# Kernel tuning notes

Measured on AMD Instinct MI355X. Metric: run time of the kernel, lower is better.

## Reference

```python
import jax, jax.numpy as jnp
import numpy as np

D_MODEL, N_HEADS, D_HEAD, N_CTX, BATCH = 1024, 16, 64, 2048, 4
SCALED = True
NEG = 1e10


def setup_inputs() -> dict:
    key = jax.random.key(0)
    k1, k2, k3, k4 = jax.random.split(key, 4)
    s = 1.0 / np.sqrt(D_MODEL)
    return {
        "x": jax.random.normal(k1, (BATCH, N_CTX, D_MODEL), dtype=jnp.float32),
        "W_K": jax.random.normal(k2, (N_HEADS, D_HEAD, D_MODEL), dtype=jnp.float32) * s,
        "W_Q": jax.random.normal(k3, (N_HEADS, D_HEAD, D_MODEL), dtype=jnp.float32) * s,
        "W_V": jax.random.normal(k4, (N_HEADS, D_HEAD, D_MODEL), dtype=jnp.float32) * s,
    }


def reference(x, W_K, W_Q, W_V):
    b, p, _ = x.shape
    k = jnp.einsum('ihd,bpd->biph', W_K, x)
    q = jnp.einsum('ihd,bpd->biph', W_Q, x)
    v = jnp.einsum('ihd,bpd->biph', W_V, x)
    # attn_scores_pre: [b, i, q, p] (query axis named q, key axis p)
    scores = jnp.einsum('biph,biqh->biqp', k, q)
    mask = jnp.tril(jnp.ones((p, p), dtype=scores.dtype))
    scores = jnp.tril(scores) - NEG * (1.0 - mask)
    if SCALED:
        scores = scores / np.sqrt(D_HEAD)
    attn = jax.nn.softmax(scores, axis=-1)
    z = jnp.einsum('biph,biqp->biqh', v, attn)  # [b, i, q, h]
    out = jnp.transpose(z, (0, 2, 1, 3)).reshape(b, p, -1)  # b q (i h)
    return out
```

## Files before the change

kernel.cpp:

```cpp
#include <hip/hip_runtime.h>
#include <stdint.h>

typedef unsigned short u16;
typedef short bf16x8 __attribute__((ext_vector_type(8)));
typedef float f32x4 __attribute__((ext_vector_type(4)));
typedef u16 u16x8 __attribute__((ext_vector_type(8)));
typedef u16 u16x4 __attribute__((ext_vector_type(4)));
typedef uint32_t u32x2 __attribute__((ext_vector_type(2)));

#define NB 4
#define NH 16
#define NP 2048
#define NDM 1024
#define KLOG2E 0.18033688011112042f

__device__ __forceinline__ u16 f2bf(float f) {
    union { float f; uint32_t u; } v; v.f = f;
    return (u16)((v.u + 0x7FFFu + ((v.u >> 16) & 1u)) >> 16);
}

__device__ __forceinline__ uint32_t cvtpk_bf16(float lo, float hi) {
    uint32_t r;
    asm("v_cvt_pk_bf16_f32 %0, %1, %2" : "=v"(r) : "v"(lo), "v"(hi));
    return r;
}

__global__ void convert_all(const float* __restrict__ x, const float* __restrict__ wq,
                            const float* __restrict__ wk, const float* __restrict__ wv,
                            u16* __restrict__ x_bf, u16* __restrict__ w_bf) {
    const int XT = NB * NP * NDM;
    const int M1 = NDM * NDM;
    int i = (blockIdx.x * blockDim.x + threadIdx.x) * 4;
    const float* src; u16* dst; float scale = 1.0f;
    if (i < XT) { src = x + i; dst = x_bf + i; }
    else {
        int j = i - XT;
        dst = w_bf + j;
        if (j < M1)          { src = wq + j;          scale = KLOG2E; }
        else if (j < 2 * M1) { src = wk + (j - M1); }
        else                 { src = wv + (j - 2 * M1); }
    }
    float4 f = *(const float4*)src;
    u16x4 o = { f2bf(f.x * scale), f2bf(f.y * scale), f2bf(f.z * scale), f2bf(f.w * scale) };
    *(u16x4*)dst = o;
}

__device__ __forceinline__ void load_lds16(const void* g, void* l) {
    __builtin_amdgcn_global_load_lds(
        (const __attribute__((address_space(1))) uint32_t*)g,
        (__attribute__((address_space(3))) uint32_t*)l,
        16, 0, 0);
}

__global__ __launch_bounds__(256) void proj_gemm(
    const u16* __restrict__ xbf, const u16* __restrict__ wbf,
    u16* __restrict__ qws, u16* __restrict__ kws, u16* __restrict__ vT)
{
    __shared__ u16 As[128 * 64];
    __shared__ u16 Bs[128 * 64];
    int tid = threadIdx.x;
    int wave = tid >> 6, lane = tid & 63;
    int g = lane >> 4, c = lane & 15;
    int wr = wave >> 1, wc = wave & 1;
    int gx = blockIdx.x, gy = blockIdx.y;
    int wsel = gy >> 3;
    int n0 = (gy & 7) * 128;
    long m0 = (long)gx * 128;
    const u16* asrc0 = xbf + m0 * 1024;
    const u16* bsrc0 = wbf + (long)wsel * (1024 * 1024) + (long)n0 * 1024;

    int lrow = lane >> 3;
    int lcol = (lane & 7) * 8;

    f32x4 acc[4][4];
    #pragma unroll
    for (int i = 0; i < 4; i++)
        #pragma unroll
        for (int j = 0; j < 4; j++) acc[i][j] = (f32x4){0.f, 0.f, 0.f, 0.f};

    for (int kt = 0; kt < 16; kt++) {
        const u16* ak = asrc0 + kt * 64;
        const u16* bk_ = bsrc0 + kt * 64;
        #pragma unroll
        for (int r = 0; r < 4; r++) {
            int ldsoff = r * 2048 + wave * 512;
            int grow = r * 32 + wave * 8 + lrow;
            load_lds16(ak + (long)grow * 1024 + lcol, &As[ldsoff]);
            load_lds16(bk_ + (long)grow * 1024 + lcol, &Bs[ldsoff]);
        }
        __syncthreads();
        #pragma unroll
        for (int ks = 0; ks < 2; ks++) {
            bf16x8 af[4], bf_[4];
            #pragma unroll
            for (int mt = 0; mt < 4; mt++)
                af[mt] = *(const bf16x8*)&As[(wr * 64 + mt * 16 + c) * 64 + ks * 32 + g * 8];
            #pragma unroll
            for (int nt = 0; nt < 4; nt++)
                bf_[nt] = *(const bf16x8*)&Bs[(wc * 64 + nt * 16 + c) * 64 + ks * 32 + g * 8];
            #pragma unroll
            for (int mt = 0; mt < 4; mt++)
                #pragma unroll
                for (int nt = 0; nt < 4; nt++)
                    acc[mt][nt] = __builtin_amdgcn_mfma_f32_16x16x32_bf16(bf_[nt], af[mt], acc[mt][nt], 0, 0, 0);
        }
        __syncthreads();
    }

    if (wsel < 2) {
        u16* dst = (wsel == 0) ? qws : kws;
        #pragma unroll
        for (int mt = 0; mt < 4; mt++) {
            #pragma unroll
            for (int nt = 0; nt < 4; nt++) {
                long m = m0 + wr * 64 + mt * 16 + c;
                int n_base = n0 + wc * 64 + nt * 16 + g * 4;
                int b = (int)(m >> 11), p = (int)(m & 2047);
                int hd = n_base >> 6, h = n_base & 63;
                u16x4 o;
                #pragma unroll
                for (int r = 0; r < 4; r++) o[r] = f2bf(acc[mt][nt][r]);
                *(u16x4*)(dst + ((((long)b * NH + hd) * NP + p) << 6) + h) = o;
            }
        }
    } else {
        #pragma unroll
        for (int mt = 0; mt < 4; mt++) {
            long m = m0 + wr * 64 + mt * 16 + c;
            int b = (int)(m >> 11), p = (int)(m & 2047);
            #pragma unroll
            for (int nt = 0; nt < 4; nt++) {
                int n_base = n0 + wc * 64 + nt * 16 + g * 4;
                #pragma unroll
                for (int r = 0; r < 4; r++)
                    vT[((long)b * 1024 + n_base + r) * NP + p] = f2bf(acc[mt][nt][r]);
            }
        }
    }
}

template<bool MASK>
__device__ __forceinline__ void attn_tile(
    int kv0, const u16* __restrict__ kp, const u16* __restrict__ vp,
    const bf16x8 (&aq)[2][2], uint8_t* PwB, int c, int g, int sx, int q0,
    f32x4 (&acc_o)[2][4], float (&lrow)[2])
{
    float ps[2] = {0.f, 0.f};
    #pragma unroll
    for (int a = 0; a < 4; a++) {
        const u16* kr = kp + (size_t)(kv0 + a * 16 + c) * 64 + g * 8;
        bf16x8 kf0 = *(const bf16x8*)(kr);
        bf16x8 kf1 = *(const bf16x8*)(kr + 32);
        #pragma unroll
        for (int mt = 0; mt < 2; mt++) {
            f32x4 z = (f32x4){0.f, 0.f, 0.f, 0.f};
            z = __builtin_amdgcn_mfma_f32_16x16x32_bf16(kf0, aq[mt][0], z, 0, 0, 0);
            z = __builtin_amdgcn_mfma_f32_16x16x32_bf16(kf1, aq[mt][1], z, 0, 0, 0);
            float p[4];
            #pragma unroll
            for (int r = 0; r < 4; r++) {
                p[r] = __builtin_amdgcn_exp2f(z[r] - 8.0f);
                if (MASK) {
                    int key = kv0 + a * 16 + g * 4 + r;
                    int qq = q0 + mt * 16 + c;
                    if (key > qq) p[r] = 0.f;
                }
                ps[mt] += p[r];
            }
            u32x2 wd = { cvtpk_bf16(p[0], p[1]), cvtpk_bf16(p[2], p[3]) };
            *(u32x2*)(PwB + (mt * 16 + c) * 128 + ((a * 32 + g * 8) ^ sx)) = wd;
        }
    }

    bf16x8 bv0[4];
    #pragma unroll
    for (int j = 0; j < 4; j++)
        bv0[j] = *(const bf16x8*)(vp + (size_t)(j * 16 + c) * NP + kv0 + g * 8);

    #pragma unroll
    for (int mt = 0; mt < 2; mt++) {
        float p = ps[mt];
        p += __shfl_xor(p, 16);
        p += __shfl_xor(p, 32);
        lrow[mt] += p;
    }

    __builtin_amdgcn_wave_barrier();

    bf16x8 pa0 = *(const bf16x8*)(PwB + (0 * 16 + c) * 128 + ((0 + g * 16) ^ sx));
    bf16x8 pa1 = *(const bf16x8*)(PwB + (1 * 16 + c) * 128 + ((0 + g * 16) ^ sx));
    bf16x8 bv1[4];
    #pragma unroll
    for (int j = 0; j < 4; j++)
        bv1[j] = *(const bf16x8*)(vp + (size_t)(j * 16 + c) * NP + kv0 + 32 + g * 8);
    #pragma unroll
    for (int j = 0; j < 4; j++) {
        acc_o[0][j] = __builtin_amdgcn_mfma_f32_16x16x32_bf16(pa0, bv0[j], acc_o[0][j], 0, 0, 0);
        acc_o[1][j] = __builtin_amdgcn_mfma_f32_16x16x32_bf16(pa1, bv0[j], acc_o[1][j], 0, 0, 0);
    }
    pa0 = *(const bf16x8*)(PwB + (0 * 16 + c) * 128 + ((64 + g * 16) ^ sx));
    pa1 = *(const bf16x8*)(PwB + (1 * 16 + c) * 128 + ((64 + g * 16) ^ sx));
    #pragma unroll
    for (int j = 0; j < 4; j++) {
        acc_o[0][j] = __builtin_amdgcn_mfma_f32_16x16x32_bf16(pa0, bv1[j], acc_o[0][j], 0, 0, 0);
        acc_o[1][j] = __builtin_amdgcn_mfma_f32_16x16x32_bf16(pa1, bv1[j], acc_o[1][j], 0, 0, 0);
    }
    __builtin_amdgcn_wave_barrier();
}

__global__ __launch_bounds__(256, 4) void attn_kernel(
    const u16* __restrict__ qws, const u16* __restrict__ kws,
    const u16* __restrict__ vT, float* __restrict__ out)
{
    __shared__ __align__(16) uint8_t Plds[16384];
    int tid = threadIdx.x;
    int wave = tid >> 6, lane = tid & 63;
    int c = lane & 15, g = lane >> 4;
    int xs = blockIdx.x >> 6;
    int qb = (xs < 4) ? (15 - xs) : (xs < 8) ? (xs + 4) : (xs < 12) ? (xs - 4) : (15 - xs);
    int bh = blockIdx.x & 63;
    int q0 = qb * 128 + wave * 32;
    const u16* qp = qws + (long)bh * NP * 64;
    const u16* kp = kws + (long)bh * NP * 64;
    const u16* vp = vT + (long)bh * 64 * NP;
    uint8_t* PwB = Plds + wave * 4096;
    int sx = ((c & 7) << 4) ^ ((c & 8) << 3);

    bf16x8 aq[2][2];
    #pragma unroll
    for (int mt = 0; mt < 2; mt++)
        #pragma unroll
        for (int s = 0; s < 2; s++)
            aq[mt][s] = *(const bf16x8*)(qp + (long)(q0 + mt * 16 + c) * 64 + s * 32 + g * 8);

    f32x4 acc_o[2][4];
    float lrow[2] = {0.f, 0.f};
    #pragma unroll
    for (int mt = 0; mt < 2; mt++)
        #pragma unroll
        for (int j = 0; j < 4; j++) acc_o[mt][j] = (f32x4){0.f, 0.f, 0.f, 0.f};

    int tmax = (q0 + 31) >> 6;
    for (int t = 0; t < tmax; t++)
        attn_tile<false>(t * 64, kp, vp, aq, PwB, c, g, sx, q0, acc_o, lrow);
    attn_tile<true>(tmax * 64, kp, vp, aq, PwB, c, g, sx, q0, acc_o, lrow);

    int b = bh >> 4, hh = bh & 15;
    #pragma unroll
    for (int mt = 0; mt < 2; mt++) {
        float invc = 1.0f / lrow[mt];
        #pragma unroll
        for (int r = 0; r < 4; r++) {
            float li = __shfl(invc, g * 4 + r);
            int qq = q0 + mt * 16 + g * 4 + r;
            #pragma unroll
            for (int j = 0; j < 4; j++)
                out[((long)b * NP + qq) * 1024 + hh * 64 + j * 16 + c] = acc_o[mt][j][r] * li;
        }
    }
}

extern "C" void kernel_launch(void* const* d_in, const int* in_sizes, int n_in,
                              void* d_out, int out_size, void* d_ws, size_t ws_size,
                              hipStream_t stream) {
    const float* x  = (const float*)d_in[0];
    const float* wk = (const float*)d_in[1];
    const float* wq = (const float*)d_in[2];
    const float* wv = (const float*)d_in[3];

    uint8_t* ws = (uint8_t*)d_ws;
    u16* x_bf = (u16*)(ws + 0);
    u16* w_bf = (u16*)(ws + (16u << 20));
    u16* q_ws = (u16*)(ws + (22u << 20));
    u16* k_ws = (u16*)(ws + (38u << 20));
    u16* v_wsT = (u16*)(ws + (54u << 20));

    convert_all<<<11264, 256, 0, stream>>>(x, wq, wk, wv, x_bf, w_bf);
    proj_gemm<<<dim3(64, 24), 256, 0, stream>>>(x_bf, w_bf, q_ws, k_ws, v_wsT);
    attn_kernel<<<1024, 256, 0, stream>>>(q_ws, k_ws, v_wsT, (float*)d_out);
}
```

Measured before the change: 227.5 us.

## Stage K tiles through triple-buffered LDS and widen attention blocks to 256 queries

The attention kernel now cooperatively loads K tiles into a three-slot LDS ring with async global-to-LDS loads. These loads are prefetched two tiles ahead and synchronised with block barriers, so K is no longer fetched per wave from global memory. Each wave handles 64 queries instead of 32, halving the grid to 512 blocks, and the row sums are computed by an extra MFMA against a ones vector instead of shuffle reductions. The wider tiles raise register use (launch bounds drop to 2 blocks per CU). Waves whose causal range ends early sit idle at the barriers until the block's last tile, which costs some load balance.

Result: faster. 186.1 us (-18.2%).

```diff
diff --git a/kernel.cpp b/kernel.cpp
--- a/kernel.cpp
+++ b/kernel.cpp
@@ -141,18 +141,17 @@
 
 template<bool MASK>
 __device__ __forceinline__ void attn_tile(
-    int kv0, const u16* __restrict__ kp, const u16* __restrict__ vp,
-    const bf16x8 (&aq)[2][2], uint8_t* PwB, int c, int g, int sx, int q0,
-    f32x4 (&acc_o)[2][4], float (&lrow)[2])
+    const uint8_t* ldsK, const bf16x8 (&bv)[2][4], const bf16x8 (&aq)[4][2],
+    const bf16x8 ones, uint8_t* PwB, int c, int g, int swz, int sx,
+    f32x4 (&acc_o)[4][4], f32x4 (&acc_l)[4])
 {
-    float ps[2] = {0.f, 0.f};
+    __builtin_amdgcn_s_setprio(1);
     #pragma unroll
     for (int a = 0; a < 4; a++) {
-        const u16* kr = kp + (size_t)(kv0 + a * 16 + c) * 64 + g * 8;
-        bf16x8 kf0 = *(const bf16x8*)(kr);
-        bf16x8 kf1 = *(const bf16x8*)(kr + 32);
-        #pragma unroll
-        for (int mt = 0; mt < 2; mt++) {
+        bf16x8 kf0 = *(const bf16x8*)(ldsK + (a * 16 + c) * 128 + ((g * 16) ^ swz));
+        bf16x8 kf1 = *(const bf16x8*)(ldsK + (a * 16 + c) * 128 + ((64 + g * 16) ^ swz));
+        #pragma unroll
+        for (int mt = 0; mt < 4; mt++) {
             f32x4 z = (f32x4){0.f, 0.f, 0.f, 0.f};
             z = __builtin_amdgcn_mfma_f32_16x16x32_bf16(kf0, aq[mt][0], z, 0, 0, 0);
             z = __builtin_amdgcn_mfma_f32_16x16x32_bf16(kf1, aq[mt][1], z, 0, 0, 0);
@@ -161,101 +160,133 @@
             for (int r = 0; r < 4; r++) {
                 p[r] = __builtin_amdgcn_exp2f(z[r] - 8.0f);
                 if (MASK) {
-                    int key = kv0 + a * 16 + g * 4 + r;
-                    int qq = q0 + mt * 16 + c;
-                    if (key > qq) p[r] = 0.f;
+                    if (a * 16 + g * 4 + r > mt * 16 + c) p[r] = 0.f;
                 }
-                ps[mt] += p[r];
             }
             u32x2 wd = { cvtpk_bf16(p[0], p[1]), cvtpk_bf16(p[2], p[3]) };
             *(u32x2*)(PwB + (mt * 16 + c) * 128 + ((a * 32 + g * 8) ^ sx)) = wd;
         }
     }
-
-    bf16x8 bv0[4];
-    #pragma unroll
-    for (int j = 0; j < 4; j++)
-        bv0[j] = *(const bf16x8*)(vp + (size_t)(j * 16 + c) * NP + kv0 + g * 8);
-
-    #pragma unroll
-    for (int mt = 0; mt < 2; mt++) {
-        float p = ps[mt];
-        p += __shfl_xor(p, 16);
-        p += __shfl_xor(p, 32);
-        lrow[mt] += p;
-    }
+    __builtin_amdgcn_s_setprio(0);
 
     __builtin_amdgcn_wave_barrier();
 
-    bf16x8 pa0 = *(const bf16x8*)(PwB + (0 * 16 + c) * 128 + ((0 + g * 16) ^ sx));
-    bf16x8 pa1 = *(const bf16x8*)(PwB + (1 * 16 + c) * 128 + ((0 + g * 16) ^ sx));
-    bf16x8 bv1[4];
-    #pragma unroll
-    for (int j = 0; j < 4; j++)
-        bv1[j] = *(const bf16x8*)(vp + (size_t)(j * 16 + c) * NP + kv0 + 32 + g * 8);
-    #pragma unroll
-    for (int j = 0; j < 4; j++) {
-        acc_o[0][j] = __builtin_amdgcn_mfma_f32_16x16x32_bf16(pa0, bv0[j], acc_o[0][j], 0, 0, 0);
-        acc_o[1][j] = __builtin_amdgcn_mfma_f32_16x16x32_bf16(pa1, bv0[j], acc_o[1][j], 0, 0, 0);
-    }
-    pa0 = *(const bf16x8*)(PwB + (0 * 16 + c) * 128 + ((64 + g * 16) ^ sx));
-    pa1 = *(const bf16x8*)(PwB + (1 * 16 + c) * 128 + ((64 + g * 16) ^ sx));
-    #pragma unroll
-    for (int j = 0; j < 4; j++) {
-        acc_o[0][j] = __builtin_amdgcn_mfma_f32_16x16x32_bf16(pa0, bv1[j], acc_o[0][j], 0, 0, 0);
-        acc_o[1][j] = __builtin_amdgcn_mfma_f32_16x16x32_bf16(pa1, bv1[j], acc_o[1][j], 0, 0, 0);
-    }
+    __builtin_amdgcn_s_setprio(1);
+    #pragma unroll
+    for (int s = 0; s < 2; s++) {
+        #pragma unroll
+        for (int mt = 0; mt < 4; mt++) {
+            bf16x8 pa = *(const bf16x8*)(PwB + (mt * 16 + c) * 128 + ((s * 64 + g * 16) ^ sx));
+            #pragma unroll
+            for (int j = 0; j < 4; j++)
+                acc_o[mt][j] = __builtin_amdgcn_mfma_f32_16x16x32_bf16(pa, bv[s][j], acc_o[mt][j], 0, 0, 0);
+            acc_l[mt] = __builtin_amdgcn_mfma_f32_16x16x32_bf16(pa, ones, acc_l[mt], 0, 0, 0);
+        }
+    }
+    __builtin_amdgcn_s_setprio(0);
     __builtin_amdgcn_wave_barrier();
 }
 
-__global__ __launch_bounds__(256, 4) void attn_kernel(
+__global__ __launch_bounds__(256, 2) void attn_kernel(
     const u16* __restrict__ qws, const u16* __restrict__ kws,
     const u16* __restrict__ vT, float* __restrict__ out)
 {
-    __shared__ __align__(16) uint8_t Plds[16384];
+    __shared__ __align__(16) uint8_t smem[57344];
     int tid = threadIdx.x;
     int wave = tid >> 6, lane = tid & 63;
     int c = lane & 15, g = lane >> 4;
     int xs = blockIdx.x >> 6;
-    int qb = (xs < 4) ? (15 - xs) : (xs < 8) ? (xs + 4) : (xs < 12) ? (xs - 4) : (15 - xs);
+    int qb = (xs < 4) ? (7 - 2 * xs) : (2 * (xs - 4));
     int bh = blockIdx.x & 63;
-    int q0 = qb * 128 + wave * 32;
+    int q0 = qb * 256 + wave * 64;
     const u16* qp = qws + (long)bh * NP * 64;
-    const u16* kp = kws + (long)bh * NP * 64;
+    const uint8_t* kb = (const uint8_t*)(kws + (long)bh * NP * 64);
     const u16* vp = vT + (long)bh * 64 * NP;
-    uint8_t* PwB = Plds + wave * 4096;
-    int sx = ((c & 7) << 4) ^ ((c & 8) << 3);
-
-    bf16x8 aq[2][2];
-    #pragma unroll
-    for (int mt = 0; mt < 2; mt++)
+    uint8_t* PwB = smem + 24576 + wave * 8192;
+    int swz = (c & 7) << 4;
+    int sx = swz ^ ((c & 8) << 3);
+
+    bf16x8 aq[4][2];
+    #pragma unroll
+    for (int mt = 0; mt < 4; mt++)
         #pragma unroll
         for (int s = 0; s < 2; s++)
             aq[mt][s] = *(const bf16x8*)(qp + (long)(q0 + mt * 16 + c) * 64 + s * 32 + g * 8);
 
-    f32x4 acc_o[2][4];
-    float lrow[2] = {0.f, 0.f};
-    #pragma unroll
-    for (int mt = 0; mt < 2; mt++)
+    bf16x8 ones;
+    #pragma unroll
+    for (int i = 0; i < 8; i++) ones[i] = (short)0x3F80;
+
+    f32x4 acc_o[4][4];
+    f32x4 acc_l[4];
+    #pragma unroll
+    for (int mt = 0; mt < 4; mt++) {
+        acc_l[mt] = (f32x4){0.f, 0.f, 0.f, 0.f};
         #pragma unroll
         for (int j = 0; j < 4; j++) acc_o[mt][j] = (f32x4){0.f, 0.f, 0.f, 0.f};
-
-    int tmax = (q0 + 31) >> 6;
-    for (int t = 0; t < tmax; t++)
-        attn_tile<false>(t * 64, kp, vp, aq, PwB, c, g, sx, q0, acc_o, lrow);
-    attn_tile<true>(tmax * 64, kp, vp, aq, PwB, c, g, sx, q0, acc_o, lrow);
+    }
+
+    int r3 = lane >> 3;
+    int cb = ((lane & 7) ^ r3) << 4;
+
+    int myTmax = q0 >> 6;
+    int Tblk = qb * 4 + 3;
+
+    auto stage = [&](int t) {
+        uint8_t* dst = smem + (t % 3) * 8192;
+        int kv = t * 64;
+        #pragma unroll
+        for (int n = 0; n < 2; n++) {
+            int row = n * 32 + wave * 8 + r3;
+            load_lds16(kb + (size_t)(kv + row) * 128 + cb, dst + n * 4096 + wave * 1024);
+        }
+    };
+
+    stage(0);
+    stage(1);
+    asm volatile("s_waitcnt vmcnt(2)" ::: "memory");
+    __builtin_amdgcn_sched_barrier(0);
+    __builtin_amdgcn_s_barrier();
+    __builtin_amdgcn_sched_barrier(0);
+
+    for (int t = 0; t <= Tblk; t++) {
+        bool active = (t <= myTmax);
+        bf16x8 bv[2][4];
+        if (active) {
+            int kv0 = t * 64;
+            #pragma unroll
+            for (int s = 0; s < 2; s++)
+                #pragma unroll
+                for (int j = 0; j < 4; j++)
+                    bv[s][j] = *(const bf16x8*)(vp + (size_t)(j * 16 + c) * NP + kv0 + s * 32 + g * 8);
+        }
+        if (t + 2 <= Tblk) stage(t + 2);
+        if (active) {
+            const uint8_t* ldsK = smem + (t % 3) * 8192;
+            if (t == myTmax)
+                attn_tile<true>(ldsK, bv, aq, ones, PwB, c, g, swz, sx, acc_o, acc_l);
+            else
+                attn_tile<false>(ldsK, bv, aq, ones, PwB, c, g, swz, sx, acc_o, acc_l);
+        }
+        if (t + 2 <= Tblk) { asm volatile("s_waitcnt vmcnt(2)" ::: "memory"); }
+        else               { asm volatile("s_waitcnt vmcnt(0)" ::: "memory"); }
+        __builtin_amdgcn_sched_barrier(0);
+        __builtin_amdgcn_s_barrier();
+        __builtin_amdgcn_sched_barrier(0);
+    }
 
     int b = bh >> 4, hh = bh & 15;
     #pragma unroll
-    for (int mt = 0; mt < 2; mt++) {
-        float invc = 1.0f / lrow[mt];
+    for (int mt = 0; mt < 4; mt++) {
+        f32x4 inv;
+        #pragma unroll
+        for (int r = 0; r < 4; r++) inv[r] = 1.0f / acc_l[mt][r];
         #pragma unroll
         for (int r = 0; r < 4; r++) {
-            float li = __shfl(invc, g * 4 + r);
             int qq = q0 + mt * 16 + g * 4 + r;
             #pragma unroll
             for (int j = 0; j < 4; j++)
-                out[((long)b * NP + qq) * 1024 + hh * 64 + j * 16 + c] = acc_o[mt][j][r] * li;
+                out[((long)b * NP + qq) * 1024 + hh * 64 + j * 16 + c] = acc_o[mt][j][r] * inv[r];
         }
     }
 }
@@ -277,5 +308,5 @@
 
     convert_all<<<11264, 256, 0, stream>>>(x, wq, wk, wv, x_bf, w_bf);
     proj_gemm<<<dim3(64, 24), 256, 0, stream>>>(x_bf, w_bf, q_ws, k_ws, v_wsT);
-    attn_kernel<<<1024, 256, 0, stream>>>(q_ws, k_ws, v_wsT, (float*)d_out);
-}
+    attn_kernel<<<512, 256, 0, stream>>>(q_ws, k_ws, v_wsT, (float*)d_out);
+}
```
